# Performance work log

Hardware: AMD Instinct MI355X
Metric: run time of the kernel (lower is better)

Reference implementation:

```python
import jax, jax.numpy as jnp
import numpy as np
from jax import lax

# dims
B, N, F = 128, 65536, 512


def setup_inputs() -> dict:
    key = jax.random.key(0)
    k1, k2 = jax.random.split(key)
    x = jax.random.normal(k1, (B, N), dtype=jnp.float32)          # dry audio
    logits = jax.random.normal(k2, (B, F, 5), dtype=jnp.float32)  # [bs, n_frames, 5]
    return {"x": x, "logits": logits}


def linear_interpolate_dim1(v, n_out):
    # v: [B, n_in, C] -> [B, n_out, C], linear interp with align_corners=True
    n_in = v.shape[1]
    pos = jnp.arange(n_out, dtype=jnp.float32) * ((n_in - 1) / (n_out - 1))
    i0 = jnp.clip(jnp.floor(pos).astype(jnp.int32), 0, n_in - 2)
    frac = (pos - i0.astype(jnp.float32))[None, :, None]
    return v[:, i0, :] * (1.0 - frac) + v[:, i0 + 1, :] * frac


def logits_to_a_coeff_triangle(a_logits):
    # stability-triangle parameterization: |a2| < 1 and |a1| < 1 + a2
    a1 = 2.0 * jnp.tanh(a_logits[..., 0])
    a1_abs = jnp.abs(a1)
    a2 = 0.5 * ((2.0 - a1_abs) * jnp.tanh(a_logits[..., 1]) + a1_abs)
    return jnp.stack([a1, a2], axis=-1)  # [B, F, 2]


def sample_wise_lpc2(x, a):
    # y[n] = x[n] - a1[n]*y[n-1] - a2[n]*y[n-2];  x: [B,N], a: [B,N,2]
    def step(carry, inp):
        y1, y2 = carry
        xn, a1, a2 = inp
        y = xn - a1 * y1 - a2 * y2
        return (y, y1), y
    z = jnp.zeros(x.shape[0], dtype=x.dtype)
    xs = (x.T, a[:, :, 0].T, a[:, :, 1].T)  # time-major
    _, ys = lax.scan(step, (z, z), xs)
    return ys.T


def time_varying_fir(x, b):
    # y[n] = b0[n]*x[n] + b1[n]*x[n-1] + b2[n]*x[n-2];  b: [B,N,3]
    xp = jnp.pad(x, ((0, 0), (2, 0)))
    return b[:, :, 0] * xp[:, 2:] + b[:, :, 1] * xp[:, 1:-1] + b[:, :, 2] * xp[:, :-2]


def reference(x, logits):
    n_samples = x.shape[1]
    # interp_logits=False: map a-logits to coeffs at frame rate, then interpolate
    a_coeff = logits_to_a_coeff_triangle(logits[..., :2])          # [B, F, 2]
    b_coeff = logits[..., 2:]                                      # [B, F, 3]
    a_coeff = linear_interpolate_dim1(a_coeff, n_samples)          # [B, N, 2]
    b_coeff = linear_interpolate_dim1(b_coeff, n_samples)          # [B, N, 3]
    y_a = sample_wise_lpc2(x, a_coeff)
    y_ab = time_varying_fir(y_a, b_coeff)
    return y_ab
```

## Files before the change

### kernel.cpp

```cpp
#include <hip/hip_runtime.h>
#include <hip/hip_bf16.h>

#define B_   128
#define N_   65536
#define F_   512
#define CS   64
#define CPR  (N_ / CS)
#define TPB  128
#define BLK_SAMP (TPB * CS)
#define NBLK (B_ * CPR / TPB)
#define KPOS ((float)(511.0 / 65535.0))
#define STRIDE 68

#define OFF_COEF   0
#define OFF_TRANS  (B_ * F_ * 5)
#define OFF_STATES (OFF_TRANS + 6 * B_ * CPR)
#define NT (B_ * CPR)

__global__ void coeff_kernel(const float* __restrict__ logits, float* __restrict__ coef) {
    int t = blockIdx.x * blockDim.x + threadIdx.x;
    if (t >= B_ * F_) return;
    const float* L = logits + (size_t)t * 5;
    float l0 = L[0], l1 = L[1], l2 = L[2], l3 = L[3], l4 = L[4];
    float a1 = 2.0f * tanhf(l0);
    float ab = fabsf(a1);
    float a2 = 0.5f * ((2.0f - ab) * tanhf(l1) + ab);
    float* C = coef + (size_t)t * 5;
    C[0] = a1; C[1] = a2; C[2] = l2; C[3] = l3; C[4] = l4;
}

__global__ __launch_bounds__(TPB) void phase1_kernel(const float* __restrict__ x,
                                                     const float* __restrict__ coef,
                                                     float* __restrict__ trans) {
    __shared__ __align__(16) float buf[TPB][STRIDE];
    int tid = threadIdx.x;
    int gchunk0 = blockIdx.x * TPB;

    const float4* xg = (const float4*)x + (size_t)gchunk0 * (CS / 4);
    #pragma unroll
    for (int it = 0; it < BLK_SAMP / 4 / TPB; ++it) {
        int i4 = it * TPB + tid;
        float4 v = xg[i4];
        int c = i4 >> 4;
        int k = (i4 & 15) * 4;
        *(float4*)&buf[c][k] = v;
    }
    __syncthreads();

    int t = gchunk0 + tid;
    int b = t >> 10;
    int c = t & (CPR - 1);
    int n0 = c * CS;

    int I  = min((int)floorf((float)n0 * KPOS), F_ - 2);
    int I2 = min(I + 2, F_ - 1);
    const float* Cb = coef + (size_t)b * F_ * 5;
    float a1A = Cb[I * 5 + 0],       a2A = Cb[I * 5 + 1];
    float a1B = Cb[(I + 1) * 5 + 0], a2B = Cb[(I + 1) * 5 + 1];
    float a1C = Cb[I2 * 5 + 0],      a2C = Cb[I2 * 5 + 1];

    float A00 = 1.f, A01 = 0.f, A10 = 0.f, A11 = 1.f, v0 = 0.f, v1 = 0.f;
    #pragma unroll 4
    for (int j = 0; j < CS / 4; ++j) {
        float4 xv = *(const float4*)&buf[tid][j * 4];
        #pragma unroll
        for (int u = 0; u < 4; ++u) {
            int k = j * 4 + u;
            float xn = (&xv.x)[u];
            float pos = (float)(n0 + k) * KPOS;
            int i0 = min((int)floorf(pos), F_ - 2);
            float frac = pos - (float)i0;
            float om = 1.0f - frac;
            bool sel = i0 > I;
            float a1 = om * (sel ? a1B : a1A) + frac * (sel ? a1C : a1B);
            float a2 = om * (sel ? a2B : a2A) + frac * (sel ? a2C : a2B);
            float nA00 = -a1 * A00 - a2 * A10;
            float nA01 = -a1 * A01 - a2 * A11;
            float nv0  = xn - a1 * v0 - a2 * v1;
            A10 = A00; A11 = A01; v1 = v0;
            A00 = nA00; A01 = nA01; v0 = nv0;
        }
    }
    trans[0 * NT + t] = A00;
    trans[1 * NT + t] = A01;
    trans[2 * NT + t] = A10;
    trans[3 * NT + t] = A11;
    trans[4 * NT + t] = v0;
    trans[5 * NT + t] = v1;
}

__global__ __launch_bounds__(1024) void scan_kernel(const float* __restrict__ trans,
                                                    float* __restrict__ states) {
    __shared__ float s0[CPR], s1[CPR], s2[CPR], s3[CPR], s4[CPR], s5[CPR];
    int b = blockIdx.x;
    int c = threadIdx.x;
    size_t base = (size_t)b * CPR + c;
    float A00 = trans[0 * NT + base], A01 = trans[1 * NT + base];
    float A10 = trans[2 * NT + base], A11 = trans[3 * NT + base];
    float v0  = trans[4 * NT + base], v1  = trans[5 * NT + base];
    for (int d = 1; d < CPR; d <<= 1) {
        s0[c] = A00; s1[c] = A01; s2[c] = A10; s3[c] = A11; s4[c] = v0; s5[c] = v1;
        __syncthreads();
        if (c >= d) {
            float f00 = s0[c - d], f01 = s1[c - d];
            float f10 = s2[c - d], f11 = s3[c - d];
            float fv0 = s4[c - d], fv1 = s5[c - d];
            float n00 = A00 * f00 + A01 * f10;
            float n01 = A00 * f01 + A01 * f11;
            float n10 = A10 * f00 + A11 * f10;
            float n11 = A10 * f01 + A11 * f11;
            float nv0 = A00 * fv0 + A01 * fv1 + v0;
            float nv1 = A10 * fv0 + A11 * fv1 + v1;
            A00 = n00; A01 = n01; A10 = n10; A11 = n11; v0 = nv0; v1 = nv1;
        }
        __syncthreads();
    }
    float* st0 = states;
    float* st1 = states + NT;
    size_t rb = (size_t)b * CPR;
    if (c == 0) { st0[rb] = 0.f; st1[rb] = 0.f; }
    if (c < CPR - 1) { st0[rb + c + 1] = v0; st1[rb + c + 1] = v1; }
}

__global__ __launch_bounds__(TPB) void phase3_kernel(const float* __restrict__ x,
                                                     const float* __restrict__ coef,
                                                     const float* __restrict__ states,
                                                     float* __restrict__ out) {
    __shared__ __align__(16) float buf[TPB][STRIDE];
    int tid = threadIdx.x;
    int gchunk0 = blockIdx.x * TPB;

    const float4* xg = (const float4*)x + (size_t)gchunk0 * (CS / 4);
    #pragma unroll
    for (int it = 0; it < BLK_SAMP / 4 / TPB; ++it) {
        int i4 = it * TPB + tid;
        float4 v = xg[i4];
        int c = i4 >> 4;
        int k = (i4 & 15) * 4;
        *(float4*)&buf[c][k] = v;
    }
    __syncthreads();

    int t = gchunk0 + tid;
    int b = t >> 10;
    int c = t & (CPR - 1);
    int n0 = c * CS;

    int I  = min((int)floorf((float)n0 * KPOS), F_ - 2);
    int I2 = min(I + 2, F_ - 1);
    const float* Cb = coef + (size_t)b * F_ * 5;
    float cA[5], cB[5], cC[5];
    #pragma unroll
    for (int j = 0; j < 5; ++j) {
        cA[j] = Cb[I * 5 + j];
        cB[j] = Cb[(I + 1) * 5 + j];
        cC[j] = Cb[I2 * 5 + j];
    }
    float s0v = states[t];
    float s1v = states[NT + t];

    #pragma unroll 4
    for (int j = 0; j < CS / 4; ++j) {
        float4 xv = *(const float4*)&buf[tid][j * 4];
        float4 yv;
        #pragma unroll
        for (int u = 0; u < 4; ++u) {
            int k = j * 4 + u;
            float xn = (&xv.x)[u];
            float pos = (float)(n0 + k) * KPOS;
            int i0 = min((int)floorf(pos), F_ - 2);
            float frac = pos - (float)i0;
            float om = 1.0f - frac;
            bool sel = i0 > I;
            float a1 = om * (sel ? cB[0] : cA[0]) + frac * (sel ? cC[0] : cB[0]);
            float a2 = om * (sel ? cB[1] : cA[1]) + frac * (sel ? cC[1] : cB[1]);
            float b0 = om * (sel ? cB[2] : cA[2]) + frac * (sel ? cC[2] : cB[2]);
            float b1 = om * (sel ? cB[3] : cA[3]) + frac * (sel ? cC[3] : cB[3]);
            float b2 = om * (sel ? cB[4] : cA[4]) + frac * (sel ? cC[4] : cB[4]);
            float y = xn - a1 * s0v - a2 * s1v;
            (&yv.x)[u] = b0 * y + b1 * s0v + b2 * s1v;
            s1v = s0v; s0v = y;
        }
        *(float4*)&buf[tid][j * 4] = yv;
    }
    __syncthreads();

    float4* og = (float4*)out + (size_t)gchunk0 * (CS / 4);
    #pragma unroll
    for (int it = 0; it < BLK_SAMP / 4 / TPB; ++it) {
        int i4 = it * TPB + tid;
        int cc = i4 >> 4;
        int k = (i4 & 15) * 4;
        og[i4] = *(float4*)&buf[cc][k];
    }
}

extern "C" void kernel_launch(void* const* d_in, const int* in_sizes, int n_in,
                              void* d_out, int out_size, void* d_ws, size_t ws_size,
                              hipStream_t stream) {
    const float* x      = (const float*)d_in[0];
    const float* logits = (const float*)d_in[1];
    float* out = (float*)d_out;
    float* ws  = (float*)d_ws;

    float* coef   = ws + OFF_COEF;
    float* trans  = ws + OFF_TRANS;
    float* states = ws + OFF_STATES;

    coeff_kernel<<<(B_ * F_ + 255) / 256, 256, 0, stream>>>(logits, coef);
    phase1_kernel<<<NBLK, TPB, 0, stream>>>(x, coef, trans);
    scan_kernel<<<B_, CPR, 0, stream>>>(trans, states);
    phase3_kernel<<<NBLK, TPB, 0, stream>>>(x, coef, states, out);
}
```

Before: 109.0 us.

## Fuse coefficient and scan stages into block-level decoupled scan with recompute

Removes the separate coefficient kernel by computing tanh-based a-coefficients inline from logits, and replaces the global per-chunk transform array plus 1024-wide scan kernel with an in-block shared-memory scan that emits one aggregate per block. A tiny kernel scans the 8 block aggregates per row, and the final kernel recomputes chunk transforms and the in-block scan to derive each chunk's starting state. This trades extra recomputation of the recurrence and tanh for less global traffic and one fewer launch.

```diff
diff --git a/kernel.cpp b/kernel.cpp
--- a/kernel.cpp
+++ b/kernel.cpp
@@ -7,32 +7,28 @@
 #define CS   64
 #define CPR  (N_ / CS)
 #define TPB  128
+#define CPB  TPB
+#define BPR  (CPR / CPB)
+#define NBLK (B_ * BPR)
 #define BLK_SAMP (TPB * CS)
-#define NBLK (B_ * CPR / TPB)
 #define KPOS ((float)(511.0 / 65535.0))
 #define STRIDE 68
 
-#define OFF_COEF   0
-#define OFF_TRANS  (B_ * F_ * 5)
-#define OFF_STATES (OFF_TRANS + 6 * B_ * CPR)
-#define NT (B_ * CPR)
-
-__global__ void coeff_kernel(const float* __restrict__ logits, float* __restrict__ coef) {
-    int t = blockIdx.x * blockDim.x + threadIdx.x;
-    if (t >= B_ * F_) return;
-    const float* L = logits + (size_t)t * 5;
-    float l0 = L[0], l1 = L[1], l2 = L[2], l3 = L[3], l4 = L[4];
-    float a1 = 2.0f * tanhf(l0);
+#define OFF_AGG   0
+#define OFF_START (NBLK * 6)
+
+__device__ __forceinline__ void load_acoef(const float* Lg, int i, float& a1, float& a2) {
+    float l0 = Lg[i * 5 + 0], l1 = Lg[i * 5 + 1];
+    a1 = 2.0f * tanhf(l0);
     float ab = fabsf(a1);
-    float a2 = 0.5f * ((2.0f - ab) * tanhf(l1) + ab);
-    float* C = coef + (size_t)t * 5;
-    C[0] = a1; C[1] = a2; C[2] = l2; C[3] = l3; C[4] = l4;
-}
-
-__global__ __launch_bounds__(TPB) void phase1_kernel(const float* __restrict__ x,
-                                                     const float* __restrict__ coef,
-                                                     float* __restrict__ trans) {
+    a2 = 0.5f * ((2.0f - ab) * tanhf(l1) + ab);
+}
+
+__global__ __launch_bounds__(TPB) void phaseA(const float* __restrict__ x,
+                                              const float* __restrict__ logits,
+                                              float* __restrict__ blockAgg) {
     __shared__ __align__(16) float buf[TPB][STRIDE];
+    __shared__ float sc[6][TPB];
     int tid = threadIdx.x;
     int gchunk0 = blockIdx.x * TPB;
 
@@ -41,9 +37,7 @@
     for (int it = 0; it < BLK_SAMP / 4 / TPB; ++it) {
         int i4 = it * TPB + tid;
         float4 v = xg[i4];
-        int c = i4 >> 4;
-        int k = (i4 & 15) * 4;
-        *(float4*)&buf[c][k] = v;
+        *(float4*)&buf[i4 >> 4][(i4 & 15) * 4] = v;
     }
     __syncthreads();
 
@@ -54,10 +48,11 @@
 
     int I  = min((int)floorf((float)n0 * KPOS), F_ - 2);
     int I2 = min(I + 2, F_ - 1);
-    const float* Cb = coef + (size_t)b * F_ * 5;
-    float a1A = Cb[I * 5 + 0],       a2A = Cb[I * 5 + 1];
-    float a1B = Cb[(I + 1) * 5 + 0], a2B = Cb[(I + 1) * 5 + 1];
-    float a1C = Cb[I2 * 5 + 0],      a2C = Cb[I2 * 5 + 1];
+    const float* Lg = logits + (size_t)b * F_ * 5;
+    float a1A, a2A, a1B, a2B, a1C, a2C;
+    load_acoef(Lg, I,     a1A, a2A);
+    load_acoef(Lg, I + 1, a1B, a2B);
+    load_acoef(Lg, I2,    a1C, a2C);
 
     float A00 = 1.f, A01 = 0.f, A10 = 0.f, A11 = 1.f, v0 = 0.f, v1 = 0.f;
     #pragma unroll 4
@@ -81,30 +76,15 @@
             A00 = nA00; A01 = nA01; v0 = nv0;
         }
     }
-    trans[0 * NT + t] = A00;
-    trans[1 * NT + t] = A01;
-    trans[2 * NT + t] = A10;
-    trans[3 * NT + t] = A11;
-    trans[4 * NT + t] = v0;
-    trans[5 * NT + t] = v1;
-}
-
-__global__ __launch_bounds__(1024) void scan_kernel(const float* __restrict__ trans,
-                                                    float* __restrict__ states) {
-    __shared__ float s0[CPR], s1[CPR], s2[CPR], s3[CPR], s4[CPR], s5[CPR];
-    int b = blockIdx.x;
-    int c = threadIdx.x;
-    size_t base = (size_t)b * CPR + c;
-    float A00 = trans[0 * NT + base], A01 = trans[1 * NT + base];
-    float A10 = trans[2 * NT + base], A11 = trans[3 * NT + base];
-    float v0  = trans[4 * NT + base], v1  = trans[5 * NT + base];
-    for (int d = 1; d < CPR; d <<= 1) {
-        s0[c] = A00; s1[c] = A01; s2[c] = A10; s3[c] = A11; s4[c] = v0; s5[c] = v1;
-        __syncthreads();
-        if (c >= d) {
-            float f00 = s0[c - d], f01 = s1[c - d];
-            float f10 = s2[c - d], f11 = s3[c - d];
-            float fv0 = s4[c - d], fv1 = s5[c - d];
+
+    for (int d = 1; d < TPB; d <<= 1) {
+        sc[0][tid] = A00; sc[1][tid] = A01; sc[2][tid] = A10;
+        sc[3][tid] = A11; sc[4][tid] = v0;  sc[5][tid] = v1;
+        __syncthreads();
+        if (tid >= d) {
+            float f00 = sc[0][tid - d], f01 = sc[1][tid - d];
+            float f10 = sc[2][tid - d], f11 = sc[3][tid - d];
+            float fv0 = sc[4][tid - d], fv1 = sc[5][tid - d];
             float n00 = A00 * f00 + A01 * f10;
             float n01 = A00 * f01 + A01 * f11;
             float n10 = A10 * f00 + A11 * f10;
@@ -115,18 +95,34 @@
         }
         __syncthreads();
     }
-    float* st0 = states;
-    float* st1 = states + NT;
-    size_t rb = (size_t)b * CPR;
-    if (c == 0) { st0[rb] = 0.f; st1[rb] = 0.f; }
-    if (c < CPR - 1) { st0[rb + c + 1] = v0; st1[rb + c + 1] = v1; }
-}
-
-__global__ __launch_bounds__(TPB) void phase3_kernel(const float* __restrict__ x,
-                                                     const float* __restrict__ coef,
-                                                     const float* __restrict__ states,
-                                                     float* __restrict__ out) {
+    if (tid == TPB - 1) {
+        float* T = blockAgg + (size_t)blockIdx.x * 6;
+        T[0] = A00; T[1] = A01; T[2] = A10; T[3] = A11; T[4] = v0; T[5] = v1;
+    }
+}
+
+__global__ __launch_bounds__(TPB) void phaseB(const float* __restrict__ blockAgg,
+                                              float* __restrict__ blockStart) {
+    int r = threadIdx.x;
+    float s0 = 0.f, s1 = 0.f;
+    #pragma unroll
+    for (int j = 0; j < BPR; ++j) {
+        int g = r * BPR + j;
+        blockStart[g * 2 + 0] = s0;
+        blockStart[g * 2 + 1] = s1;
+        const float* T = blockAgg + (size_t)g * 6;
+        float n0 = T[0] * s0 + T[1] * s1 + T[4];
+        float n1 = T[2] * s0 + T[3] * s1 + T[5];
+        s0 = n0; s1 = n1;
+    }
+}
+
+__global__ __launch_bounds__(TPB) void phaseC(const float* __restrict__ x,
+                                              const float* __restrict__ logits,
+                                              const float* __restrict__ blockStart,
+                                              float* __restrict__ out) {
     __shared__ __align__(16) float buf[TPB][STRIDE];
+    __shared__ float sc[6][TPB];
     int tid = threadIdx.x;
     int gchunk0 = blockIdx.x * TPB;
 
@@ -135,9 +131,7 @@
     for (int it = 0; it < BLK_SAMP / 4 / TPB; ++it) {
         int i4 = it * TPB + tid;
         float4 v = xg[i4];
-        int c = i4 >> 4;
-        int k = (i4 & 15) * 4;
-        *(float4*)&buf[c][k] = v;
+        *(float4*)&buf[i4 >> 4][(i4 & 15) * 4] = v;
     }
     __syncthreads();
 
@@ -148,16 +142,76 @@
 
     int I  = min((int)floorf((float)n0 * KPOS), F_ - 2);
     int I2 = min(I + 2, F_ - 1);
-    const float* Cb = coef + (size_t)b * F_ * 5;
+    const float* Lg = logits + (size_t)b * F_ * 5;
     float cA[5], cB[5], cC[5];
-    #pragma unroll
-    for (int j = 0; j < 5; ++j) {
-        cA[j] = Cb[I * 5 + j];
-        cB[j] = Cb[(I + 1) * 5 + j];
-        cC[j] = Cb[I2 * 5 + j];
-    }
-    float s0v = states[t];
-    float s1v = states[NT + t];
+    load_acoef(Lg, I,     cA[0], cA[1]);
+    load_acoef(Lg, I + 1, cB[0], cB[1]);
+    load_acoef(Lg, I2,    cC[0], cC[1]);
+    #pragma unroll
+    for (int j = 0; j < 3; ++j) {
+        cA[2 + j] = Lg[I * 5 + 2 + j];
+        cB[2 + j] = Lg[(I + 1) * 5 + 2 + j];
+        cC[2 + j] = Lg[I2 * 5 + 2 + j];
+    }
+
+    float A00 = 1.f, A01 = 0.f, A10 = 0.f, A11 = 1.f, v0 = 0.f, v1 = 0.f;
+    #pragma unroll 4
+    for (int j = 0; j < CS / 4; ++j) {
+        float4 xv = *(const float4*)&buf[tid][j * 4];
+        #pragma unroll
+        for (int u = 0; u < 4; ++u) {
+            int k = j * 4 + u;
+            float xn = (&xv.x)[u];
+            float pos = (float)(n0 + k) * KPOS;
+            int i0 = min((int)floorf(pos), F_ - 2);
+            float frac = pos - (float)i0;
+            float om = 1.0f - frac;
+            bool sel = i0 > I;
+            float a1 = om * (sel ? cB[0] : cA[0]) + frac * (sel ? cC[0] : cB[0]);
+            float a2 = om * (sel ? cB[1] : cA[1]) + frac * (sel ? cC[1] : cB[1]);
+            float nA00 = -a1 * A00 - a2 * A10;
+            float nA01 = -a1 * A01 - a2 * A11;
+            float nv0  = xn - a1 * v0 - a2 * v1;
+            A10 = A00; A11 = A01; v1 = v0;
+            A00 = nA00; A01 = nA01; v0 = nv0;
+        }
+    }
+
+    for (int d = 1; d < TPB; d <<= 1) {
+        sc[0][tid] = A00; sc[1][tid] = A01; sc[2][tid] = A10;
+        sc[3][tid] = A11; sc[4][tid] = v0;  sc[5][tid] = v1;
+        __syncthreads();
+        if (tid >= d) {
+            float f00 = sc[0][tid - d], f01 = sc[1][tid - d];
+            float f10 = sc[2][tid - d], f11 = sc[3][tid - d];
+            float fv0 = sc[4][tid - d], fv1 = sc[5][tid - d];
+            float n00 = A00 * f00 + A01 * f10;
+            float n01 = A00 * f01 + A01 * f11;
+            float n10 = A10 * f00 + A11 * f10;
+            float n11 = A10 * f01 + A11 * f11;
+            float nv0 = A00 * fv0 + A01 * fv1 + v0;
+            float nv1 = A10 * fv0 + A11 * fv1 + v1;
+            A00 = n00; A01 = n01; A10 = n10; A11 = n11; v0 = nv0; v1 = nv1;
+        }
+        __syncthreads();
+    }
+    sc[0][tid] = A00; sc[1][tid] = A01; sc[2][tid] = A10;
+    sc[3][tid] = A11; sc[4][tid] = v0;  sc[5][tid] = v1;
+    __syncthreads();
+
+    float bs0 = blockStart[(size_t)blockIdx.x * 2 + 0];
+    float bs1 = blockStart[(size_t)blockIdx.x * 2 + 1];
+    float s0v, s1v;
+    if (tid == 0) {
+        s0v = bs0; s1v = bs1;
+    } else {
+        float L00 = sc[0][tid - 1], L01 = sc[1][tid - 1];
+        float L10 = sc[2][tid - 1], L11 = sc[3][tid - 1];
+        float Lv0 = sc[4][tid - 1], Lv1 = sc[5][tid - 1];
+        s0v = L00 * bs0 + L01 * bs1 + Lv0;
+        s1v = L10 * bs0 + L11 * bs1 + Lv1;
+    }
+    __syncthreads();
 
     #pragma unroll 4
     for (int j = 0; j < CS / 4; ++j) {
@@ -189,9 +243,7 @@
     #pragma unroll
     for (int it = 0; it < BLK_SAMP / 4 / TPB; ++it) {
         int i4 = it * TPB + tid;
-        int cc = i4 >> 4;
-        int k = (i4 & 15) * 4;
-        og[i4] = *(float4*)&buf[cc][k];
+        og[i4] = *(float4*)&buf[i4 >> 4][(i4 & 15) * 4];
     }
 }
 
@@ -203,12 +255,10 @@
     float* out = (float*)d_out;
     float* ws  = (float*)d_ws;
 
-    float* coef   = ws + OFF_COEF;
-    float* trans  = ws + OFF_TRANS;
-    float* states = ws + OFF_STATES;
-
-    coeff_kernel<<<(B_ * F_ + 255) / 256, 256, 0, stream>>>(logits, coef);
-    phase1_kernel<<<NBLK, TPB, 0, stream>>>(x, coef, trans);
-    scan_kernel<<<B_, CPR, 0, stream>>>(trans, states);
-    phase3_kernel<<<NBLK, TPB, 0, stream>>>(x, coef, states, out);
-}
+    float* blockAgg   = ws + OFF_AGG;
+    float* blockStart = ws + OFF_START;
+
+    phaseA<<<NBLK, TPB, 0, stream>>>(x, logits, blockAgg);
+    phaseB<<<1, TPB, 0, stream>>>(blockAgg, blockStart);
+    phaseC<<<NBLK, TPB, 0, stream>>>(x, logits, blockStart, out);
+}
```

New measurement: 109.8 us. About the same (+0.8%).
